# Optimization experiments

Measured on AMD Instinct MI355X. Metric: run time of the kernel, lower is better.

Reference implementation:

```python
import jax, jax.numpy as jnp
import numpy as np
from jax import lax

D_MODEL = 1024
D_INNER = 2 * D_MODEL          # expand=2
D_STATE = 16
D_CONV = 4
DT_RANK = 64                   # ceil(1024/16)
DT_MIN = 0.001
DT_MAX = 0.1
BATCH = 4
SEQ = 2048


def setup_inputs() -> dict:
    key = jax.random.key(0)
    ks = jax.random.split(key, 8)
    s = lambda fan_in: 1.0 / np.sqrt(fan_in)
    x = jax.random.normal(ks[0], (BATCH, SEQ, D_MODEL), dtype=jnp.float32)
    # Linear weights stored as (in, out) so y = x @ W
    W_in = jax.random.uniform(ks[1], (D_MODEL, 2 * D_INNER), jnp.float32, -s(D_MODEL), s(D_MODEL))
    conv_w = jax.random.uniform(ks[2], (D_INNER, 1, D_CONV), jnp.float32, -s(D_CONV), s(D_CONV))
    conv_b = jax.random.uniform(ks[3], (D_INNER,), jnp.float32, -s(D_CONV), s(D_CONV))
    W_x = jax.random.uniform(ks[4], (D_INNER, DT_RANK + 2 * D_STATE), jnp.float32, -s(D_INNER), s(D_INNER))
    W_dt = jax.random.uniform(ks[5], (DT_RANK, D_INNER), jnp.float32, -s(DT_RANK), s(DT_RANK))
    b_dt = jax.random.uniform(ks[6], (D_INNER,), jnp.float32, -s(DT_RANK), s(DT_RANK))
    # A = arange(1..d_state) repeated over d_inner; store log(A)
    A_log = jnp.log(jnp.broadcast_to(jnp.arange(1, D_STATE + 1, dtype=jnp.float32), (D_INNER, D_STATE)))
    D_param = jnp.ones((D_INNER,), dtype=jnp.float32)
    W_out = jax.random.uniform(ks[7], (D_INNER, D_MODEL), jnp.float32, -s(D_INNER), s(D_INNER))
    return {"x": x, "W_in": W_in, "conv_w": conv_w, "conv_b": conv_b,
            "W_x": W_x, "W_dt": W_dt, "b_dt": b_dt, "A_log": A_log,
            "D_param": D_param, "W_out": W_out}


def reference(x, W_in, conv_w, conv_b, W_x, W_dt, b_dt, A_log, D_param, W_out):
    # in_proj + split
    xz = x @ W_in                                   # (B, S, 2*d_inner)
    x_branch, z_branch = jnp.split(xz, 2, axis=-1)  # each (B, S, d_inner)

    # causal depthwise conv1d (torch pads d_conv-1 both sides then slices [:seq])
    xc = jnp.pad(x_branch.transpose(0, 2, 1), ((0, 0), (0, 0), (D_CONV - 1, 0)))
    xc = lax.conv_general_dilated(xc, conv_w, (1,), 'VALID',
                                  dimension_numbers=('NCH', 'OIH', 'NCH'),
                                  feature_group_count=D_INNER)
    xc = xc + conv_b[None, :, None]
    x_conv = jax.nn.silu(xc.transpose(0, 2, 1))     # (B, S, d_inner)

    # input-dependent dt, B, C
    x_dbl = x_conv @ W_x                            # (B, S, dt_rank + 2*d_state)
    dt_low = x_dbl[..., :DT_RANK]
    Bm = x_dbl[..., DT_RANK:DT_RANK + D_STATE]      # (B, S, d_state)
    Cm = x_dbl[..., DT_RANK + D_STATE:]             # (B, S, d_state)
    dt = jax.nn.sigmoid(dt_low @ W_dt + b_dt) * (DT_MAX - DT_MIN) + DT_MIN
    dt = jnp.maximum(dt, 1e-4)                      # (B, S, d_inner)

    A = -jnp.exp(A_log)                             # (d_inner, d_state)

    # selective scan over time (n_substeps = 1)
    def step(h, inp):
        dt_t, B_t, C_t, x_t = inp                   # (B,di), (B,ds), (B,ds), (B,di)
        dA = jnp.exp(dt_t[:, :, None] * A[None])    # (B, di, ds)
        h = dA * h + (dt_t * x_t)[:, :, None] * B_t[:, None, :]
        y_t = jnp.sum(h * C_t[:, None, :], axis=-1) # (B, di)
        return h, y_t

    h0 = jnp.zeros((x.shape[0], D_INNER, D_STATE), dtype=x.dtype)
    _, ys = lax.scan(step, h0,
                     (dt.swapaxes(0, 1), Bm.swapaxes(0, 1),
                      Cm.swapaxes(0, 1), x_conv.swapaxes(0, 1)))
    y = ys.swapaxes(0, 1)                           # (B, S, d_inner)

    y = y + x_conv * D_param
    y = y * jax.nn.silu(z_branch)
    return y @ W_out                                # (B, S, d_model)
```

## Files before the change

kernel.cpp:

```cpp
#include <hip/hip_runtime.h>

typedef unsigned short u16;
typedef unsigned int u32;
typedef __attribute__((ext_vector_type(8))) short short8;
typedef __attribute__((ext_vector_type(4))) float f32x4;

#define NBATCH 4
#define NSEQ   2048
#define DMODEL 1024
#define DINNER 2048
#define DSTATE 16
#define DTRANK 64
#define ROWS   (NBATCH*NSEQ)
#define NCH    32
#define CLEN   64

__device__ __forceinline__ float b2f(u16 u){ union{u32 i; float f;} v; v.i=((u32)u)<<16; return v.f; }
__device__ __forceinline__ u16 f2b(float f){ union{float f; u32 i;} v; v.f=f; u32 i=v.i; return (u16)((i + 0x7FFFu + ((i>>16)&1u))>>16); }
__device__ __forceinline__ float sigmoidf_(float x){ return 1.0f/(1.0f+__expf(-x)); }

__global__ __launch_bounds__(256) void prep(const u16* __restrict__ x,
    const u16* __restrict__ Win, const u16* __restrict__ convw,
    const u16* __restrict__ Wx, const u16* __restrict__ Wdt,
    const u16* __restrict__ Alog, const u16* __restrict__ Wout,
    const u16* __restrict__ v0, const u16* __restrict__ v1, const u16* __restrict__ v2,
    int* __restrict__ meta){
  __shared__ int vote;
  __shared__ int mxbits;
  const int tid = threadIdx.x;
  const u16* V[3] = {v0, v1, v2};

  const u16* ptrs[6] = {x, Win, convw, Wx, Wdt, Wout};
  const float bounds[6] = {8.f, 0.045f, 0.6f, 0.035f, 0.15f, 0.035f};
  const int slots[6] = {0, 1, 2, 4, 5, 9};
  for (int q = 0; q < 6; q++){
    if (tid == 0) vote = 1;
    __syncthreads();
    int bad = 0;
    for (int i = tid; i < 2048; i += 256){
      float v = fabsf(b2f(ptrs[q][i]));
      if (!(v <= bounds[q])) bad = 1;
    }
    if (bad) atomicAnd(&vote, 0);
    __syncthreads();
    if (tid == 0) meta[slots[q]] = vote;
    __syncthreads();
  }
  if (tid == 0){ u16 u = Alog[1]; meta[7] = (u == 0x3F31 || u == 0x3F32) ? 1 : 0; }

  int iD = -1, fD = 1;
  for (int k = 0; k < 3; k++){
    if (V[k][0] == 0x3F80 && V[k][1] == 0x3F80){ iD = k; fD = 1; }
    else if (V[k][0] == 0 && V[k][1] == 0x3F80 && V[k][2] == 0){ iD = k; fD = 0; }
  }
  if (iD < 0){ iD = 2; fD = 1; }
  int oo[2], no = 0;
  for (int k = 0; k < 3; k++) if (k != iD) oo[no++] = k;
  int fo[2]; float mo[2];
  for (int q = 0; q < 2; q++){
    if (tid == 0) vote = 1;
    __syncthreads();
    int bad = 0;
    for (int i = tid; i < 2048; i += 256){
      float v = fabsf(b2f(V[oo[q]][i]));
      if (!(v <= 0.6f)) bad = 1;
    }
    if (bad) atomicAnd(&vote, 0);
    __syncthreads();
    fo[q] = vote;
    if (tid == 0) mxbits = 0;
    __syncthreads();
    float m = 0.f;
    for (int i = tid; i < 2048; i += 256){
      float v = fabsf(fo[q] ? b2f(V[oo[q]][i]) : ((const float*)V[oo[q]])[i]);
      m = fmaxf(m, v);
    }
    atomicMax(&mxbits, __float_as_int(m));
    __syncthreads();
    mo[q] = __int_as_float(mxbits);
    __syncthreads();
  }
  if (tid == 0){
    int a = (mo[0] > 0.25f) ? 0 : 1;
    meta[10] = oo[a];     meta[3] = fo[a];
    meta[11] = oo[1-a];   meta[6] = fo[1-a];
    meta[12] = iD;        meta[8] = fD;
  }
}

__global__ __launch_bounds__(256) void cvt_bf16(const void* __restrict__ in,
                                                u16* __restrict__ out, long n,
                                                const int* __restrict__ meta, int slot){
  long i = (long)blockIdx.x*256 + threadIdx.x;
  if (i >= n) return;
  if (meta[slot]) out[i] = ((const u16*)in)[i];
  else            out[i] = f2b(((const float*)in)[i]);
}

__global__ __launch_bounds__(256) void cvt_trio(const void* __restrict__ v0,
                                                const void* __restrict__ v1,
                                                const void* __restrict__ v2,
                                                const int* __restrict__ meta,
                                                u16* __restrict__ cbc,
                                                u16* __restrict__ bdtc,
                                                u16* __restrict__ dpc){
  int i = blockIdx.x*256 + threadIdx.x;
  int which = i >> 11, d = i & 2047;
  const void* V[3] = {v0, v1, v2};
  int src, fl; u16* dst;
  if (which == 0){ src = meta[10]; fl = meta[3]; dst = cbc; }
  else if (which == 1){ src = meta[11]; fl = meta[6]; dst = bdtc; }
  else { src = meta[12]; fl = meta[8]; dst = dpc; }
  dst[d] = fl ? ((const u16*)V[src])[d] : f2b(((const float*)V[src])[d]);
}

__global__ __launch_bounds__(256) void transpose_pad(const void* __restrict__ inv,
                                                     u16* __restrict__ out,
                                                     int K, int N, int Nout,
                                                     const int* __restrict__ meta, int slot){
  __shared__ u16 t[32][33];
  const int f = meta[slot];
  const u16*   ib = (const u16*)inv;
  const float* iff = (const float*)inv;
  int k0 = blockIdx.x*32, n0 = blockIdx.y*32;
  int tx = threadIdx.x & 31, ty = threadIdx.x >> 5;
  #pragma unroll
  for (int i=0;i<32;i+=8){
    int k = k0+ty+i, n = n0+tx;
    u16 v = 0;
    if (k<K && n<N) v = f ? ib[(long)k*N+n] : f2b(iff[(long)k*N+n]);
    t[ty+i][tx] = v;
  }
  __syncthreads();
  #pragma unroll
  for (int i=0;i<32;i+=8){
    int n = n0+ty+i, k = k0+tx;
    if (n<Nout && k<K) out[(long)n*K+k] = t[tx][ty+i];
  }
}

template<int MODE>
__global__ __launch_bounds__(256) void gemm_bt(
    const u16* __restrict__ A, int lda,
    const u16* __restrict__ Bt, int K,
    u16* __restrict__ C0, u16* __restrict__ C1, int ldc,
    const u16* __restrict__ bias, float* __restrict__ Cf)
{
  __shared__ u16 sa[128*64];
  __shared__ u16 sb[128*64];
  const int tid = threadIdx.x;
  const int lane = tid & 63;
  const int wave = tid >> 6;
  const int wm = (wave >> 1) * 64;
  const int wn = (wave & 1) * 64;
  const int lane15 = lane & 15;
  const int quad = lane >> 4;
  const long rowBase = (long)blockIdx.y * 128;
  const long colBase = (long)blockIdx.x * 128;

  f32x4 acc[4][4];
  #pragma unroll
  for (int i=0;i<4;i++)
    #pragma unroll
    for (int j=0;j<4;j++)
      #pragma unroll
      for (int r=0;r<4;r++) acc[i][j][r]=0.0f;

  const int e  = tid*8;
  const int r0 = e >> 6;
  const int c0 = e & 63;

  for (int kb=0; kb<K; kb+=64) {
    #pragma unroll
    for (int i=0;i<4;i++){
      const u16* ga = A + (rowBase + r0 + i*32)*lda + kb + c0;
      __builtin_amdgcn_global_load_lds((const __attribute__((address_space(1))) void*)ga,
                                       (__attribute__((address_space(3))) void*)&sa[e + i*2048],
                                       16, 0, 0);
    }
    #pragma unroll
    for (int i=0;i<4;i++){
      const u16* gb = Bt + (colBase + r0 + i*32)*(long)K + kb + c0;
      __builtin_amdgcn_global_load_lds((const __attribute__((address_space(1))) void*)gb,
                                       (__attribute__((address_space(3))) void*)&sb[e + i*2048],
                                       16, 0, 0);
    }
    __syncthreads();
    #pragma unroll
    for (int ko=0; ko<2; ko++){
      const int kk = ko*32 + quad*8;
      short8 af[4], bfr[4];
      #pragma unroll
      for (int i=0;i<4;i++) af[i]  = *(const short8*)&sa[(wm + i*16 + lane15)*64 + kk];
      #pragma unroll
      for (int j=0;j<4;j++) bfr[j] = *(const short8*)&sb[(wn + j*16 + lane15)*64 + kk];
      #pragma unroll
      for (int i=0;i<4;i++)
        #pragma unroll
        for (int j=0;j<4;j++)
          acc[i][j] = __builtin_amdgcn_mfma_f32_16x16x32_bf16(af[i], bfr[j], acc[i][j], 0, 0, 0);
    }
    __syncthreads();
  }

  #pragma unroll
  for (int i=0;i<4;i++){
    #pragma unroll
    for (int j=0;j<4;j++){
      long row = rowBase + wm + i*16 + quad*4;
      long col = colBase + wn + j*16 + lane15;
      #pragma unroll
      for (int r=0;r<4;r++){
        float v = acc[i][j][r];
        long rr = row + r;
        if (MODE == 0) {
          C0[rr*ldc + col] = f2b(v);
        } else if (MODE == 2) {
          float t  = sigmoidf_(v + b2f(bias[col]));
          float dv = fmaxf(t*0.099f + 0.001f, 1e-4f);
          C0[rr*ldc + col] = f2b(dv);
        }
      }
    }
  }
}

template<int MODE>
__global__ __launch_bounds__(512, 2) void gemm256(
    const u16* __restrict__ A, int lda,
    const u16* __restrict__ Bt, int K,
    u16* __restrict__ C0, u16* __restrict__ C1, int ldc,
    float* __restrict__ Cf)
{
  __shared__ u16 sa[2*16384];
  __shared__ u16 sb[2*16384];
  const int tid  = threadIdx.x;
  const int lane = tid & 63;
  const int wm   = (tid >> 6) >> 2;
  const int wn   = (tid >> 6) & 3;
  const int lane15 = lane & 15;
  const int quad   = lane >> 4;

  const int nwg  = gridDim.x * gridDim.y;
  const int orig = blockIdx.y * gridDim.x + blockIdx.x;
  const int swz  = (orig & 7) * (nwg >> 3) + (orig >> 3);
  const int bx   = swz % gridDim.x;
  const int by   = swz / gridDim.x;
  const long rowBase = (long)by * 256;
  const long colBase = (long)bx * 256;

  const int xorv = (lane15 & 7) << 3;
  const int k0   = (quad*8) ^ xorv;
  const int k1   = (32 + quad*8) ^ xorv;
  const int aBase = (wm*128 + lane15) * 64;
  const int bBase = (wn*64  + lane15) * 64;

  const int scol = ((tid & 7) ^ ((tid >> 3) & 7)) << 3;
  const int arow = tid >> 3;
  const int bsub = ((tid >> 8) & 1)*64 + ((tid & 255) >> 3);
  const int bdst = (tid & 7) * 8;

  f32x4 acc[8][4];
  #pragma unroll
  for (int i=0;i<8;i++)
    #pragma unroll
    for (int j=0;j<4;j++)
      #pragma unroll
      for (int r=0;r<4;r++) acc[i][j][r]=0.0f;

  const int nt = K >> 6;

  auto stageA = [&](int buf, int rs, int kb){
    const u16* g = A + (rowBase + rs + arow)*(long)lda + kb + scol;
    __builtin_amdgcn_global_load_lds((const __attribute__((address_space(1))) void*)g,
        (__attribute__((address_space(3))) void*)&sa[buf*16384 + rs*64 + tid*8], 16, 0, 0);
  };
  auto stageB = [&](int buf, int cq, int part, int kb){
    const int row = part*128 + cq*32 + bsub;
    const u16* g = Bt + (colBase + row)*(long)K + kb + scol;
    __builtin_amdgcn_global_load_lds((const __attribute__((address_space(1))) void*)g,
        (__attribute__((address_space(3))) void*)&sb[buf*16384 + row*64 + bdst], 16, 0, 0);
  };

  stageA(0,   0, 0); stageA(0, 128, 0);
  stageB(0, 0, 0, 0); stageB(0, 0, 1, 0);
  stageA(0,  64, 0); stageA(0, 192, 0);
  stageB(0, 1, 0, 0); stageB(0, 1, 1, 0);
  asm volatile("s_waitcnt vmcnt(4)\n\ts_barrier" ::: "memory");

  for (int t = 0; t < nt; ++t){
    const int cur = t & 1, nb = cur ^ 1;
    const int kb2 = (t+1) << 6;
    const bool pf = (t+1 < nt);
    const u16* sA = &sa[cur*16384];
    const u16* sB = &sb[cur*16384];
    short8 a0[4][2], a1[4][2], b0[2][2], b1[2][2];

    #pragma unroll
    for (int i=0;i<4;i++){
      a0[i][0] = *(const short8*)&sA[aBase + i*1024 + k0];
      a0[i][1] = *(const short8*)&sA[aBase + i*1024 + k1];
    }
    #pragma unroll
    for (int j=0;j<2;j++){
      b0[j][0] = *(const short8*)&sB[bBase + j*1024 + k0];
      b0[j][1] = *(const short8*)&sB[bBase + j*1024 + k1];
    }
    if (pf){ stageA(nb, 0, kb2); stageA(nb, 128, kb2); }
    __builtin_amdgcn_s_setprio(1);
    #pragma unroll
    for (int s=0;s<2;s++)
      #pragma unroll
      for (int i=0;i<4;i++)
        #pragma unroll
        for (int j=0;j<2;j++)
          acc[i][j] = __builtin_amdgcn_mfma_f32_16x16x32_bf16(a0[i][s], b0[j][s], acc[i][j], 0, 0, 0);
    __builtin_amdgcn_s_setprio(0);
    asm volatile("s_waitcnt vmcnt(4)\n\ts_barrier" ::: "memory");

    #pragma unroll
    for (int i=0;i<4;i++){
      a1[i][0] = *(const short8*)&sA[aBase + 4096 + i*1024 + k0];
      a1[i][1] = *(const short8*)&sA[aBase + 4096 + i*1024 + k1];
    }
    if (pf){ stageB(nb, 0, 0, kb2); stageB(nb, 0, 1, kb2); }
    __builtin_amdgcn_s_setprio(1);
    #pragma unroll
    for (int s=0;s<2;s++)
      #pragma unroll
      for (int i=0;i<4;i++)
        #pragma unroll
        for (int j=0;j<2;j++)
          acc[4+i][j] = __builtin_amdgcn_mfma_f32_16x16x32_bf16(a1[i][s], b0[j][s], acc[4+i][j], 0, 0, 0);
    __builtin_amdgcn_s_setprio(0);
    asm volatile("s_waitcnt vmcnt(4)\n\ts_barrier" ::: "memory");

    #pragma unroll
    for (int j=0;j<2;j++){
      b1[j][0] = *(const short8*)&sB[bBase + 2048 + j*1024 + k0];
      b1[j][1] = *(const short8*)&sB[bBase + 2048 + j*1024 + k1];
    }
    if (pf){ stageA(nb, 64, kb2); stageA(nb, 192, kb2); }
    __builtin_amdgcn_s_setprio(1);
    #pragma unroll
    for (int s=0;s<2;s++)
      #pragma unroll
      for (int i=0;i<4;i++)
        #pragma unroll
        for (int j=0;j<2;j++)
          acc[i][2+j] = __builtin_amdgcn_mfma_f32_16x16x32_bf16(a0[i][s], b1[j][s], acc[i][2+j], 0, 0, 0);
    __builtin_amdgcn_s_setprio(0);
    asm volatile("s_barrier" ::: "memory");

    if (pf){ stageB(nb, 1, 0, kb2); stageB(nb, 1, 1, kb2); }
    __builtin_amdgcn_s_setprio(1);
    #pragma unroll
    for (int s=0;s<2;s++)
      #pragma unroll
      for (int i=0;i<4;i++)
        #pragma unroll
        for (int j=0;j<2;j++)
          acc[4+i][2+j] = __builtin_amdgcn_mfma_f32_16x16x32_bf16(a1[i][s], b1[j][s], acc[4+i][2+j], 0, 0, 0);
    __builtin_amdgcn_s_setprio(0);
    asm volatile("s_waitcnt vmcnt(4)\n\ts_barrier" ::: "memory");
  }

  #pragma unroll
  for (int i=0;i<8;i++){
    const long row = rowBase + wm*128 + i*16 + quad*4;
    #pragma unroll
    for (int j=0;j<4;j++){
      const long col = colBase + wn*64 + j*16 + lane15;
      #pragma unroll
      for (int r=0;r<4;r++){
        const float v = acc[i][j][r];
        const long rr = row + r;
        if (MODE == 1){
          if (col < 2048) C0[rr*2048 + col] = f2b(v);
          else            C1[rr*2048 + (col-2048)] = f2b(v);
        } else {
          Cf[rr*ldc + col] = v;
        }
      }
    }
  }
}

__global__ __launch_bounds__(256) void conv_silu(const u16* __restrict__ xb,
                                                 const u16* __restrict__ w,
                                                 const u16* __restrict__ bias,
                                                 u16* __restrict__ xc){
  long idx8 = ((long)blockIdx.x*256 + threadIdx.x) * 8;
  int d = (int)(idx8 & (DINNER-1));
  int s = (int)((idx8 >> 11) & (NSEQ-1));
  int b = (int)(idx8 >> 22);

  short8 bv = *(const short8*)(bias + d);
  short8 wv0 = *(const short8*)(w + d*4);
  short8 wv1 = *(const short8*)(w + d*4 + 8);
  short8 wv2 = *(const short8*)(w + d*4 + 16);
  short8 wv3 = *(const short8*)(w + d*4 + 24);
  u16 wl[32];
  #pragma unroll
  for (int q=0;q<8;q++){ wl[q] = ((u16*)&wv0)[q]; wl[8+q] = ((u16*)&wv1)[q];
                         wl[16+q] = ((u16*)&wv2)[q]; wl[24+q] = ((u16*)&wv3)[q]; }

  float acc[8];
  #pragma unroll
  for (int l=0;l<8;l++) acc[l] = b2f(((u16*)&bv)[l]);

  #pragma unroll
  for (int j=0;j<4;j++){
    int t = s - 3 + j;
    if (t >= 0){
      short8 xv = *(const short8*)(xb + ((long)(b*NSEQ + t))*DINNER + d);
      #pragma unroll
      for (int l=0;l<8;l++)
        acc[l] += b2f(((u16*)&xv)[l]) * b2f(wl[l*4 + j]);
    }
  }
  short8 ov;
  #pragma unroll
  for (int l=0;l<8;l++){ float y = acc[l]*sigmoidf_(acc[l]); ((u16*)&ov)[l] = f2b(y); }
  *(short8*)(xc + idx8) = ov;
}

__global__ __launch_bounds__(256) void scan_pass1(const u16* __restrict__ dt,
                                                  const u16* __restrict__ xc,
                                                  const u16* __restrict__ xdbl,
                                                  const u16* __restrict__ Alog,
                                                  float* __restrict__ hend,
                                                  float* __restrict__ sumdt){
  int d = blockIdx.x*256 + threadIdx.x;
  int c = blockIdx.y;
  int b = blockIdx.z;
  __shared__ float sB[CLEN][DSTATE];
  for (int i=threadIdx.x; i<CLEN*DSTATE; i+=256){
    int t = i >> 4, s = i & 15;
    sB[t][s] = b2f(xdbl[((long)(b*NSEQ + c*CLEN + t))*128 + DTRANK + s]);
  }
  float Acf[DSTATE];
  #pragma unroll
  for (int s=0;s<DSTATE;s++) Acf[s] = -__expf(b2f(Alog[d*DSTATE + s]));
  __syncthreads();

  float h[DSTATE];
  #pragma unroll
  for (int s=0;s<DSTATE;s++) h[s] = 0.0f;
  float sd = 0.0f;
  long base = ((long)(b*NSEQ + c*CLEN))*DINNER + d;
  for (int t=0;t<CLEN;t++){
    float dtv = b2f(dt[base + (long)t*DINNER]);
    float xv  = b2f(xc[base + (long)t*DINNER]);
    float u = dtv*xv;
    sd += dtv;
    #pragma unroll
    for (int s=0;s<DSTATE;s++){
      float dA = __expf(dtv * Acf[s]);
      h[s] = dA*h[s] + u*sB[t][s];
    }
  }
  long hidx = ((long)(b*DINNER + d)*NCH + c)*DSTATE;
  #pragma unroll
  for (int s=0;s<DSTATE;s++) hend[hidx + s] = h[s];
  sumdt[(long)(b*DINNER + d)*NCH + c] = sd;
}

__global__ __launch_bounds__(256) void scan_pass2(float* __restrict__ hend,
                                                  const float* __restrict__ sumdt,
                                                  const u16* __restrict__ Alog){
  long i = (long)blockIdx.x*256 + threadIdx.x;
  int s = (int)(i & 15);
  long bd = i >> 4;
  int d = (int)(bd & (DINNER-1));
  float A = -__expf(b2f(Alog[d*DSTATE + s]));
  float run = 0.0f;
  long base = bd*NCH*DSTATE + s;
  for (int c=0;c<NCH;c++){
    float e = hend[base + (long)c*DSTATE];
    float decay = __expf(A * sumdt[bd*NCH + c]);
    hend[base + (long)c*DSTATE] = run;
    run = run*decay + e;
  }
}

__global__ __launch_bounds__(256) void scan_pass3(const u16* __restrict__ dt,
                                                  u16* __restrict__ xc,
                                                  const u16* __restrict__ zb,
                                                  const u16* __restrict__ xdbl,
                                                  const u16* __restrict__ Alog,
                                                  const u16* __restrict__ Dp,
                                                  const float* __restrict__ hstart){
  int d = blockIdx.x*256 + threadIdx.x;
  int c = blockIdx.y;
  int b = blockIdx.z;
  __shared__ float sB[CLEN][DSTATE];
  __shared__ float sC[CLEN][DSTATE];
  for (int i=threadIdx.x; i<CLEN*DSTATE; i+=256){
    int t = i >> 4, s = i & 15;
    long rb = ((long)(b*NSEQ + c*CLEN + t))*128;
    sB[t][s] = b2f(xdbl[rb + DTRANK + s]);
    sC[t][s] = b2f(xdbl[rb + DTRANK + DSTATE + s]);
  }
  float Acf[DSTATE];
  #pragma unroll
  for (int s=0;s<DSTATE;s++) Acf[s] = -__expf(b2f(Alog[d*DSTATE + s]));
  __syncthreads();

  float h[DSTATE];
  long hidx = ((long)(b*DINNER + d)*NCH + c)*DSTATE;
  #pragma unroll
  for (int s=0;s<DSTATE;s++) h[s] = hstart[hidx + s];
  float Dpv = b2f(Dp[d]);
  long base = ((long)(b*NSEQ + c*CLEN))*DINNER + d;
  for (int t=0;t<CLEN;t++){
    float dtv = b2f(dt[base + (long)t*DINNER]);
    float xv  = b2f(xc[base + (long)t*DINNER]);
    float zv  = b2f(zb[base + (long)t*DINNER]);
    float u = dtv*xv;
    float y = 0.0f;
    #pragma unroll
    for (int s=0;s<DSTATE;s++){
      float dA = __expf(dtv * Acf[s]);
      h[s] = dA*h[s] + u*sB[t][s];
      y += h[s]*sC[t][s];
    }
    y += xv * Dpv;
    y *= zv * sigmoidf_(zv);
    xc[base + (long)t*DINNER] = f2b(y);
  }
}

extern "C" void kernel_launch(void* const* d_in, const int* in_sizes, int n_in,
                              void* d_out, int out_size, void* d_ws, size_t ws_size,
                              hipStream_t stream) {
  const void *x=nullptr,*W_in=nullptr,*conv_w=nullptr,*W_x=nullptr,*W_dt=nullptr,
             *A_log=nullptr,*W_out=nullptr;
  const void* v2048[3] = {nullptr,nullptr,nullptr};
  int n2048 = 0;
  for (int i = 0; i < n_in; i++){
    switch (in_sizes[i]){
      case 8388608: x      = d_in[i]; break;
      case 4194304: W_in   = d_in[i]; break;
      case 8192:    conv_w = d_in[i]; break;
      case 196608:  W_x    = d_in[i]; break;
      case 131072:  W_dt   = d_in[i]; break;
      case 32768:   A_log  = d_in[i]; break;
      case 2097152: W_out  = d_in[i]; break;
      case 2048:    if (n2048 < 3) v2048[n2048++] = d_in[i]; break;
      default: break;
    }
  }

  size_t off = 0;
  char* wsb = (char*)d_ws;
  auto take = [&](size_t n){ void* p = wsb + off; off += (n + 255) & ~(size_t)255; return p; };
  u16* Wt_in  = (u16*)take((size_t)4096*1024*2);
  u16* Wt_x   = (u16*)take((size_t)128*2048*2);
  u16* Wt_dt  = (u16*)take((size_t)2048*64*2);
  u16* Wt_out = (u16*)take((size_t)1024*2048*2);
  u16* xb     = (u16*)take((size_t)ROWS*DINNER*2);
  u16* zb     = (u16*)take((size_t)ROWS*DINNER*2);
  u16* xc     = (u16*)take((size_t)ROWS*DINNER*2);
  u16* xdbl   = (u16*)take((size_t)ROWS*128*2);
  char* shr = (char*)take((size_t)ROWS*NCH*DSTATE*4 + (size_t)ROWS*NCH*4 + 4096);
  u16*   xcvt  = (u16*)shr;
  float* hend  = (float*)shr;
  float* sumdt = (float*)(shr + (size_t)ROWS*NCH*DSTATE*4);
  u16* cwc  = (u16*)take(DINNER*4*2);
  u16* cbc  = (u16*)take(DINNER*2);
  u16* bdtc = (u16*)take(DINNER*2);
  u16* alc  = (u16*)take(DINNER*DSTATE*2);
  u16* dpc  = (u16*)take(DINNER*2);
  int* meta = (int*)take(256);
  u16* dtb = xb;

  prep<<<1, 256, 0, stream>>>((const u16*)x, (const u16*)W_in, (const u16*)conv_w,
                              (const u16*)W_x, (const u16*)W_dt, (const u16*)A_log,
                              (const u16*)W_out,
                              (const u16*)v2048[0], (const u16*)v2048[1], (const u16*)v2048[2],
                              meta);

  cvt_bf16<<<(ROWS*DMODEL)/256, 256, 0, stream>>>(x, xcvt, (long)ROWS*DMODEL, meta, 0);
  cvt_bf16<<<32, 256, 0, stream>>>(conv_w, cwc, DINNER*4, meta, 2);
  cvt_bf16<<<128,256, 0, stream>>>(A_log, alc, DINNER*DSTATE, meta, 7);
  cvt_trio<<<24, 256, 0, stream>>>(v2048[0], v2048[1], v2048[2], meta, cbc, bdtc, dpc);

  transpose_pad<<<dim3(32,128), 256, 0, stream>>>(W_in, Wt_in, 1024, 4096, 4096, meta, 1);
  transpose_pad<<<dim3(64,4),   256, 0, stream>>>(W_x,  Wt_x,  2048, 96,   128,  meta, 4);
  transpose_pad<<<dim3(2,64),   256, 0, stream>>>(W_dt, Wt_dt, 64,   2048, 2048, meta, 5);
  transpose_pad<<<dim3(64,32),  256, 0, stream>>>(W_out,Wt_out,2048, 1024, 1024, meta, 9);

  gemm256<1><<<dim3(16,32), 512, 0, stream>>>(xcvt, 1024, Wt_in, 1024, xb, zb, 2048, nullptr);

  conv_silu<<<(ROWS*DINNER)/(256*8), 256, 0, stream>>>(xb, cwc, cbc, xc);

  gemm_bt<0><<<dim3(1,64), 256, 0, stream>>>(xc, 2048, Wt_x, 2048, xdbl, nullptr, 128, nullptr, nullptr);

  gemm_bt<2><<<dim3(16,64), 256, 0, stream>>>(xdbl, 128, Wt_dt, 64, dtb, nullptr, 2048, bdtc, nullptr);

  scan_pass1<<<dim3(8,NCH,NBATCH), 256, 0, stream>>>(dtb, xc, xdbl, alc, hend, sumdt);
  scan_pass2<<<(ROWS*DSTATE)/256, 256, 0, stream>>>(hend, sumdt, alc);
  scan_pass3<<<dim3(8,NCH,NBATCH), 256, 0, stream>>>(dtb, xc, zb, xdbl, alc, dpc, hend);

  gemm256<3><<<dim3(4,32), 512, 0, stream>>>(xc, 2048, Wt_out, 2048, nullptr, nullptr, 1024, (float*)d_out);
}
```

Measured before the change: 530.5 us.

## Use exp-power recurrence for integer A, shorter scan chunks, prefetch, gemm_bt out_proj

The scan kernels check at runtime whether A equals -(s+1). If so, they replace the 16 per-step exponentials with one exp(-dt) raised to successive powers by repeated multiplication. The scan also prefetches the next timestep's inputs, loads B and C with vector reads from shared memory, and halves the chunk length so twice as many chunks run in parallel. The output projection moves from gemm256 to gemm_bt with an fp32 store mode. The fast path depends on the A_log values matching the arange initialization, and the shorter chunks add more pass2 work.

```diff
diff --git a/kernel.cpp b/kernel.cpp
--- a/kernel.cpp
+++ b/kernel.cpp
@@ -12,8 +12,8 @@
 #define DSTATE 16
 #define DTRANK 64
 #define ROWS   (NBATCH*NSEQ)
-#define NCH    32
-#define CLEN   64
+#define NCH    64
+#define CLEN   32
 
 __device__ __forceinline__ float b2f(u16 u){ union{u32 i; float f;} v; v.i=((u32)u)<<16; return v.f; }
 __device__ __forceinline__ u16 f2b(float f){ union{float f; u32 i;} v; v.f=f; u32 i=v.i; return (u16)((i + 0x7FFFu + ((i>>16)&1u))>>16); }
@@ -219,6 +219,8 @@
           float t  = sigmoidf_(v + b2f(bias[col]));
           float dv = fmaxf(t*0.099f + 0.001f, 1e-4f);
           C0[rr*ldc + col] = f2b(dv);
+        } else if (MODE == 3) {
+          Cf[rr*ldc + col] = v;
         }
       }
     }
@@ -440,8 +442,12 @@
     sB[t][s] = b2f(xdbl[((long)(b*NSEQ + c*CLEN + t))*128 + DTRANK + s]);
   }
   float Acf[DSTATE];
-  #pragma unroll
-  for (int s=0;s<DSTATE;s++) Acf[s] = -__expf(b2f(Alog[d*DSTATE + s]));
+  bool fast = true;
+  #pragma unroll
+  for (int s=0;s<DSTATE;s++){
+    Acf[s] = -__expf(b2f(Alog[d*DSTATE + s]));
+    fast = fast && (fabsf(Acf[s] + (float)(s+1)) < 0.03f*(float)(s+1));
+  }
   __syncthreads();
 
   float h[DSTATE];
@@ -449,15 +455,47 @@
   for (int s=0;s<DSTATE;s++) h[s] = 0.0f;
   float sd = 0.0f;
   long base = ((long)(b*NSEQ + c*CLEN))*DINNER + d;
-  for (int t=0;t<CLEN;t++){
-    float dtv = b2f(dt[base + (long)t*DINNER]);
-    float xv  = b2f(xc[base + (long)t*DINNER]);
-    float u = dtv*xv;
-    sd += dtv;
-    #pragma unroll
-    for (int s=0;s<DSTATE;s++){
-      float dA = __expf(dtv * Acf[s]);
-      h[s] = dA*h[s] + u*sB[t][s];
+  float dtv = b2f(dt[base]);
+  float xv  = b2f(xc[base]);
+  if (fast){
+    for (int t=0;t<CLEN;t++){
+      long nxt = base + (long)((t+1<CLEN)?(t+1):t)*DINNER;
+      float dtn = b2f(dt[nxt]);
+      float xn  = b2f(xc[nxt]);
+      float B[DSTATE];
+      *(f32x4*)&B[0]  = *(const f32x4*)&sB[t][0];
+      *(f32x4*)&B[4]  = *(const f32x4*)&sB[t][4];
+      *(f32x4*)&B[8]  = *(const f32x4*)&sB[t][8];
+      *(f32x4*)&B[12] = *(const f32x4*)&sB[t][12];
+      float u = dtv*xv;
+      sd += dtv;
+      float e1 = __expf(-dtv);
+      float p = e1;
+      #pragma unroll
+      for (int s=0;s<DSTATE;s++){
+        h[s] = fmaf(p, h[s], u*B[s]);
+        p *= e1;
+      }
+      dtv = dtn; xv = xn;
+    }
+  } else {
+    for (int t=0;t<CLEN;t++){
+      long nxt = base + (long)((t+1<CLEN)?(t+1):t)*DINNER;
+      float dtn = b2f(dt[nxt]);
+      float xn  = b2f(xc[nxt]);
+      float B[DSTATE];
+      *(f32x4*)&B[0]  = *(const f32x4*)&sB[t][0];
+      *(f32x4*)&B[4]  = *(const f32x4*)&sB[t][4];
+      *(f32x4*)&B[8]  = *(const f32x4*)&sB[t][8];
+      *(f32x4*)&B[12] = *(const f32x4*)&sB[t][12];
+      float u = dtv*xv;
+      sd += dtv;
+      #pragma unroll
+      for (int s=0;s<DSTATE;s++){
+        float dA = __expf(dtv * Acf[s]);
+        h[s] = fmaf(dA, h[s], u*B[s]);
+      }
+      dtv = dtn; xv = xn;
     }
   }
   long hidx = ((long)(b*DINNER + d)*NCH + c)*DSTATE;
@@ -503,8 +541,12 @@
     sC[t][s] = b2f(xdbl[rb + DTRANK + DSTATE + s]);
   }
   float Acf[DSTATE];
-  #pragma unroll
-  for (int s=0;s<DSTATE;s++) Acf[s] = -__expf(b2f(Alog[d*DSTATE + s]));
+  bool fast = true;
+  #pragma unroll
+  for (int s=0;s<DSTATE;s++){
+    Acf[s] = -__expf(b2f(Alog[d*DSTATE + s]));
+    fast = fast && (fabsf(Acf[s] + (float)(s+1)) < 0.03f*(float)(s+1));
+  }
   __syncthreads();
 
   float h[DSTATE];
@@ -513,21 +555,69 @@
   for (int s=0;s<DSTATE;s++) h[s] = hstart[hidx + s];
   float Dpv = b2f(Dp[d]);
   long base = ((long)(b*NSEQ + c*CLEN))*DINNER + d;
-  for (int t=0;t<CLEN;t++){
-    float dtv = b2f(dt[base + (long)t*DINNER]);
-    float xv  = b2f(xc[base + (long)t*DINNER]);
-    float zv  = b2f(zb[base + (long)t*DINNER]);
-    float u = dtv*xv;
-    float y = 0.0f;
-    #pragma unroll
-    for (int s=0;s<DSTATE;s++){
-      float dA = __expf(dtv * Acf[s]);
-      h[s] = dA*h[s] + u*sB[t][s];
-      y += h[s]*sC[t][s];
-    }
-    y += xv * Dpv;
-    y *= zv * sigmoidf_(zv);
-    xc[base + (long)t*DINNER] = f2b(y);
+  float dtv = b2f(dt[base]);
+  float xv  = b2f(xc[base]);
+  float zv  = b2f(zb[base]);
+  if (fast){
+    for (int t=0;t<CLEN;t++){
+      long nxt = base + (long)((t+1<CLEN)?(t+1):t)*DINNER;
+      float dtn = b2f(dt[nxt]);
+      float xn  = b2f(xc[nxt]);
+      float zn  = b2f(zb[nxt]);
+      float B[DSTATE], C[DSTATE];
+      *(f32x4*)&B[0]  = *(const f32x4*)&sB[t][0];
+      *(f32x4*)&B[4]  = *(const f32x4*)&sB[t][4];
+      *(f32x4*)&B[8]  = *(const f32x4*)&sB[t][8];
+      *(f32x4*)&B[12] = *(const f32x4*)&sB[t][12];
+      *(f32x4*)&C[0]  = *(const f32x4*)&sC[t][0];
+      *(f32x4*)&C[4]  = *(const f32x4*)&sC[t][4];
+      *(f32x4*)&C[8]  = *(const f32x4*)&sC[t][8];
+      *(f32x4*)&C[12] = *(const f32x4*)&sC[t][12];
+      float u = dtv*xv;
+      float e1 = __expf(-dtv);
+      float gate = zv*sigmoidf_(zv);
+      float p = e1;
+      float y = 0.0f;
+      #pragma unroll
+      for (int s=0;s<DSTATE;s++){
+        h[s] = fmaf(p, h[s], u*B[s]);
+        y = fmaf(h[s], C[s], y);
+        p *= e1;
+      }
+      y = fmaf(xv, Dpv, y);
+      y *= gate;
+      xc[base + (long)t*DINNER] = f2b(y);
+      dtv = dtn; xv = xn; zv = zn;
+    }
+  } else {
+    for (int t=0;t<CLEN;t++){
+      long nxt = base + (long)((t+1<CLEN)?(t+1):t)*DINNER;
+      float dtn = b2f(dt[nxt]);
+      float xn  = b2f(xc[nxt]);
+      float zn  = b2f(zb[nxt]);
+      float B[DSTATE], C[DSTATE];
+      *(f32x4*)&B[0]  = *(const f32x4*)&sB[t][0];
+      *(f32x4*)&B[4]  = *(const f32x4*)&sB[t][4];
+      *(f32x4*)&B[8]  = *(const f32x4*)&sB[t][8];
+      *(f32x4*)&B[12] = *(const f32x4*)&sB[t][12];
+      *(f32x4*)&C[0]  = *(const f32x4*)&sC[t][0];
+      *(f32x4*)&C[4]  = *(const f32x4*)&sC[t][4];
+      *(f32x4*)&C[8]  = *(const f32x4*)&sC[t][8];
+      *(f32x4*)&C[12] = *(const f32x4*)&sC[t][12];
+      float u = dtv*xv;
+      float gate = zv*sigmoidf_(zv);
+      float y = 0.0f;
+      #pragma unroll
+      for (int s=0;s<DSTATE;s++){
+        float dA = __expf(dtv * Acf[s]);
+        h[s] = fmaf(dA, h[s], u*B[s]);
+        y = fmaf(h[s], C[s], y);
+      }
+      y = fmaf(xv, Dpv, y);
+      y *= gate;
+      xc[base + (long)t*DINNER] = f2b(y);
+      dtv = dtn; xv = xn; zv = zn;
+    }
   }
 }
 
@@ -603,5 +693,5 @@
   scan_pass2<<<(ROWS*DSTATE)/256, 256, 0, stream>>>(hend, sumdt, alc);
   scan_pass3<<<dim3(8,NCH,NBATCH), 256, 0, stream>>>(dtb, xc, zb, xdbl, alc, dpc, hend);
 
-  gemm256<3><<<dim3(4,32), 512, 0, stream>>>(xc, 2048, Wt_out, 2048, nullptr, nullptr, 1024, (float*)d_out);
-}
+  gemm_bt<3><<<dim3(8,64), 256, 0, stream>>>(xc, 2048, Wt_out, 2048, nullptr, nullptr, 1024, nullptr, (float*)d_out);
+}
```

Result: faster. 476.4 us (-10.2%).
